# Kernel tuning notes

Hardware: AMD Instinct MI355X
Metric: run time of the kernel (lower is better)

Reference implementation:

```python
import jax, jax.numpy as jnp
import numpy as np

HIGH, LOW = 768, 384
LOW2 = LOW // 2  # PNL uses low_dim // reduc_ratio, reduc_ratio=2
B, N = 8, 4096
EPS = 1e-5


def _nl_block(x_h, x_l, wg, bg, wt, bt, wp, bp, ww, bw, gamma, beta):
    # x_h: [B,N,H], x_l: [B,N0,H]; conv1x1 == per-token linear
    Nl = x_l.shape[1]
    g = jnp.einsum('bnc,dc->bnd', x_l, wg) + bg      # [B,N0,D]
    th = jnp.einsum('bnc,dc->bnd', x_h, wt) + bt     # [B,N,D]
    ph = jnp.einsum('bnc,dc->bnd', x_l, wp) + bp     # [B,N0,D]
    # attention = (th @ ph^T) / N0; y = attention @ g. Reassociate:
    kv = jnp.einsum('bnd,bne->bde', ph, g) / Nl      # [B,D,D]
    y = jnp.einsum('bnd,bde->bne', th, kv)           # [B,N,D]
    y = jnp.einsum('bnd,cd->bnc', y, ww) + bw        # [B,N,H]
    # BatchNorm1d over channel dim, training-mode batch stats (biased var)
    mu = y.mean(axis=(0, 1))
    var = y.var(axis=(0, 1))
    y = (y - mu) * jax.lax.rsqrt(var + EPS) * gamma + beta
    return y + x_h


def setup_inputs() -> dict:
    key = jax.random.key(0)
    ks = jax.random.split(key, 24)
    s = 0.02
    d = {
        'x': jax.random.normal(ks[0], (B, N, HIGH), jnp.float32),
        'x0': jax.random.normal(ks[1], (B, N, HIGH), jnp.float32),
        # CNL params (low_dim = 384)
        'c_wg': s * jax.random.normal(ks[2], (LOW, HIGH)), 'c_bg': s * jax.random.normal(ks[3], (LOW,)),
        'c_wt': s * jax.random.normal(ks[4], (LOW, HIGH)), 'c_bt': s * jax.random.normal(ks[5], (LOW,)),
        'c_wp': s * jax.random.normal(ks[6], (LOW, HIGH)), 'c_bp': s * jax.random.normal(ks[7], (LOW,)),
        'c_ww': s * jax.random.normal(ks[8], (HIGH, LOW)), 'c_bw': s * jax.random.normal(ks[9], (HIGH,)),
        'c_gamma': 1.0 + 0.1 * jax.random.normal(ks[10], (HIGH,)),
        'c_beta': s * jax.random.normal(ks[11], (HIGH,)),
        # PNL params (low_dim // 2 = 192)
        'p_wg': s * jax.random.normal(ks[12], (LOW2, HIGH)), 'p_bg': s * jax.random.normal(ks[13], (LOW2,)),
        'p_wt': s * jax.random.normal(ks[14], (LOW2, HIGH)), 'p_bt': s * jax.random.normal(ks[15], (LOW2,)),
        'p_wp': s * jax.random.normal(ks[16], (LOW2, HIGH)), 'p_bp': s * jax.random.normal(ks[17], (LOW2,)),
        'p_ww': s * jax.random.normal(ks[18], (HIGH, LOW2)), 'p_bw': s * jax.random.normal(ks[19], (HIGH,)),
        'p_gamma': 1.0 + 0.1 * jax.random.normal(ks[20], (HIGH,)),
        'p_beta': s * jax.random.normal(ks[21], (HIGH,)),
    }
    return d


def reference(x, x0,
              c_wg, c_bg, c_wt, c_bt, c_wp, c_bp, c_ww, c_bw, c_gamma, c_beta,
              p_wg, p_bg, p_wt, p_bt, p_wp, p_bp, p_ww, p_bw, p_gamma, p_beta):
    z = _nl_block(x, x0, c_wg, c_bg, c_wt, c_bt, c_wp, c_bp, c_ww, c_bw, c_gamma, c_beta)
    out = _nl_block(z, x0, p_wg, p_bg, p_wt, p_bt, p_wp, p_bp, p_ww, p_bw, p_gamma, p_beta)
    return out
```

## Files before the change

kernel.cpp:

```cpp
#include <hip/hip_runtime.h>
#include <stdint.h>

typedef unsigned short u16;
typedef __bf16 bf16x8 __attribute__((ext_vector_type(8)));
typedef short s16x8 __attribute__((ext_vector_type(8)));
typedef short s16x4 __attribute__((ext_vector_type(4)));
typedef float f32x4 __attribute__((ext_vector_type(4)));

__device__ __forceinline__ u16 f2bf(float f) {
  uint32_t u = __builtin_bit_cast(uint32_t, f);
  u += 0x7fffu + ((u >> 16) & 1u);
  return (u16)(u >> 16);
}
__device__ __forceinline__ float bf2f(u16 h) {
  uint32_t u = ((uint32_t)h) << 16;
  return __builtin_bit_cast(float, u);
}

__device__ __forceinline__ void gl16(const u16* g, u16* l) {
  __builtin_amdgcn_global_load_lds(
      (const __attribute__((address_space(1))) void*)g,
      (__attribute__((address_space(3))) void*)l, 16, 0, 0);
}

__device__ __forceinline__ void barf() {
  asm volatile("s_barrier" ::: "memory");
}

__device__ __forceinline__ int src_chunk(int l) {
  return (((l & 3) ^ ((l >> 3) & 3)) * 8);
}
__device__ __forceinline__ int rd_koff(int l) {
  return (((l >> 4) ^ (((l & 15) >> 1) & 3)) * 8);
}

__global__ void cvt_in2(const float* __restrict__ a, const float* __restrict__ b,
                        u16* __restrict__ da, u16* __restrict__ db, long n8each) {
  long stride = (long)gridDim.x * blockDim.x;
  long total = 2 * n8each;
  for (long i = (long)blockIdx.x * blockDim.x + threadIdx.x; i < total; i += stride) {
    const float* src = (i < n8each) ? a + i * 8 : b + (i - n8each) * 8;
    u16* dst = (i < n8each) ? da + i * 8 : db + (i - n8each) * 8;
    const f32x4* s = (const f32x4*)src;
    f32x4 v0 = s[0], v1 = s[1];
    s16x8 o;
#pragma unroll
    for (int j = 0; j < 4; ++j) o[j] = (short)f2bf(v0[j]);
#pragma unroll
    for (int j = 0; j < 4; ++j) o[4 + j] = (short)f2bf(v1[j]);
    *(s16x8*)dst = o;
  }
}

__global__ void cvt_flat8(const float* __restrict__ src, u16* __restrict__ dst,
                          long n8, float scale) {
  long stride = (long)gridDim.x * blockDim.x;
  for (long i = (long)blockIdx.x * blockDim.x + threadIdx.x; i < n8; i += stride) {
    const f32x4* s = (const f32x4*)(src + i * 8);
    f32x4 a = s[0], b = s[1];
    s16x8 o;
#pragma unroll
    for (int j = 0; j < 4; ++j) o[j] = (short)f2bf(a[j] * scale);
#pragma unroll
    for (int j = 0; j < 4; ++j) o[4 + j] = (short)f2bf(b[j] * scale);
    *(s16x8*)(dst + i * 8) = o;
  }
}

__global__ void prep_w(const float* __restrict__ c_wg, const float* __restrict__ c_wp,
                       const float* __restrict__ p_wg, const float* __restrict__ p_wp,
                       const float* __restrict__ c_wt, const float* __restrict__ p_wt,
                       const float* __restrict__ c_ww, const float* __restrict__ p_ww,
                       u16* __restrict__ wcat, u16* __restrict__ wt_c,
                       u16* __restrict__ wt_p, u16* __restrict__ ww_c,
                       u16* __restrict__ ww_p) {
  const int C0 = 1280 * 768 / 4;
  const int C1 = C0 + 384 * 768 / 4;
  const int C2 = C1 + 256 * 768 / 4;
  const int C3 = C2 + 768 * 384 / 4;
  const int C4 = C3 + 768 * 256 / 4;
  int stride = gridDim.x * blockDim.x;
  for (int i = blockIdx.x * blockDim.x + threadIdx.x; i < C4; i += stride) {
    const float* src = nullptr;
    u16* dst;
    if (i < C0) {
      int e = i * 4;
      dst = wcat + e;
      int r = e / 768;
      if (r < 384) src = c_wg + e;
      else if (r < 768) src = c_wp + e - 384 * 768;
      else if (r < 960) src = p_wg + e - 768 * 768;
      else if (r < 1024) src = nullptr;
      else if (r < 1216) src = p_wp + e - 1024 * 768;
      else src = nullptr;
    } else if (i < C1) {
      int e = (i - C0) * 4; dst = wt_c + e; src = c_wt + e;
    } else if (i < C2) {
      int e = (i - C1) * 4; dst = wt_p + e;
      src = (e / 768 < 192) ? p_wt + e : nullptr;
    } else if (i < C3) {
      int e = (i - C2) * 4; dst = ww_c + e; src = c_ww + e;
    } else {
      int e = (i - C3) * 4; dst = ww_p + e;
      int r = e >> 8, c = e & 255;
      src = (c < 192) ? p_ww + r * 192 + c : nullptr;
    }
    s16x4 o;
    if (src) {
      f32x4 v = *(const f32x4*)src;
#pragma unroll
      for (int j = 0; j < 4; ++j) o[j] = (short)f2bf(v[j]);
    } else {
      o = s16x4{0, 0, 0, 0};
    }
    *(s16x4*)dst = o;
  }
}

__global__ void prep_b(const float* __restrict__ c_bg, const float* __restrict__ c_bp,
                       const float* __restrict__ p_bg, const float* __restrict__ p_bp,
                       const float* __restrict__ c_bt, const float* __restrict__ p_bt,
                       float* __restrict__ biasb, float* __restrict__ sums) {
  int i = blockIdx.x * blockDim.x + threadIdx.x;
  if (i < 1920) {
    float v = 0.f;
    if (i < 384) v = c_bg[i];
    else if (i < 768) v = c_bp[i - 384];
    else if (i < 960) v = p_bg[i - 768];
    else if (i < 1024) v = 0.f;
    else if (i < 1216) v = p_bp[i - 1024];
    else if (i < 1280) v = 0.f;
    else if (i < 1664) v = c_bt[i - 1280];
    else if (i < 1856) v = p_bt[i - 1664];
    biasb[i] = v;
  } else if (i < 1920 + 3072) {
    sums[i - 1920] = 0.f;
  }
}

template <int BIAS, int SUMS>
__global__ __launch_bounds__(512) void gemm_nt_big(
    const u16* __restrict__ A, const u16* __restrict__ B, void* __restrict__ Cv,
    const float* __restrict__ bias, float* __restrict__ sums,
    int ntiles, long lda, long ldb, long ldc, int K,
    long aBatch, long bBatch, long cBatch) {
  __shared__ u16 As[4][256 * 32];
  __shared__ u16 Bs[4][256 * 32];

  const int bm = blockIdx.x / ntiles;
  const int bn = blockIdx.x % ntiles;
  const int bb = blockIdx.y;
  const int nt = K >> 5;

  const u16* Ab = A + (long)bb * aBatch + (long)bm * 256 * lda;
  const u16* Bb = B + (long)bb * bBatch + (long)bn * 256 * ldb;

  const int t = threadIdx.x;
  const int w = t >> 6;
  const int l = t & 63;
  const int wr = w >> 2;
  const int wc = w & 3;

  const int srow = w * 16 + (l >> 2);
  const int cg = src_chunk(l);
  const long aoff0 = (long)srow * lda + cg;
  const long aoff1 = (long)(128 + srow) * lda + cg;
  const long boff0 = (long)srow * ldb + cg;
  const long boff1 = (long)(128 + srow) * ldb + cg;

#define STAGE_A(T, BUF)                                   \
  gl16(Ab + aoff0 + (long)(T) * 32, &As[BUF][w * 512]);   \
  gl16(Ab + aoff1 + (long)(T) * 32, &As[BUF][(8 + w) * 512]);
#define STAGE_B(T, BUF)                                   \
  gl16(Bb + boff0 + (long)(T) * 32, &Bs[BUF][w * 512]);   \
  gl16(Bb + boff1 + (long)(T) * 32, &Bs[BUF][(8 + w) * 512]);

  f32x4 acc[8][4] = {};

  STAGE_A(0, 0); STAGE_B(0, 0);
  if (nt > 1) { STAGE_A(1, 1); STAGE_B(1, 1); }
  if (nt > 2) { STAGE_A(2, 2); STAGE_B(2, 2); }
  if (nt > 2)      asm volatile("s_waitcnt vmcnt(8)" ::: "memory");
  else if (nt > 1) asm volatile("s_waitcnt vmcnt(4)" ::: "memory");
  else             asm volatile("s_waitcnt vmcnt(0)" ::: "memory");
  barf();

  const int koff = rd_koff(l);
  const int ar = wr * 128 + (l & 15);
  const int br = wc * 64 + (l & 15);

  for (int tt = 0; tt < nt; ++tt) {
    const int cur = tt & 3;
    const int pf = (tt + 3) & 3;
    const bool do_pf = (tt + 3) < nt;

    bf16x8 bfr[4], af[4];
#pragma unroll
    for (int ni = 0; ni < 4; ++ni)
      bfr[ni] = __builtin_bit_cast(
          bf16x8, *(const s16x8*)(&Bs[cur][(br + ni * 16) * 32 + koff]));
#pragma unroll
    for (int mi = 0; mi < 4; ++mi)
      af[mi] = __builtin_bit_cast(
          bf16x8, *(const s16x8*)(&As[cur][(ar + mi * 16) * 32 + koff]));
    if (do_pf) { STAGE_A(tt + 3, pf); }
    barf();
    __builtin_amdgcn_s_setprio(1);
#pragma unroll
    for (int mi = 0; mi < 4; ++mi)
#pragma unroll
      for (int ni = 0; ni < 4; ++ni)
        acc[mi][ni] = __builtin_amdgcn_mfma_f32_16x16x32_bf16(
            af[mi], bfr[ni], acc[mi][ni], 0, 0, 0);
    __builtin_amdgcn_s_setprio(0);
    barf();

    bf16x8 ag[4];
#pragma unroll
    for (int mi = 0; mi < 4; ++mi)
      ag[mi] = __builtin_bit_cast(
          bf16x8, *(const s16x8*)(&As[cur][(ar + 64 + mi * 16) * 32 + koff]));
    if (do_pf) { STAGE_B(tt + 3, pf); }
    barf();
    __builtin_amdgcn_s_setprio(1);
#pragma unroll
    for (int mi = 0; mi < 4; ++mi)
#pragma unroll
      for (int ni = 0; ni < 4; ++ni)
        acc[4 + mi][ni] = __builtin_amdgcn_mfma_f32_16x16x32_bf16(
            ag[mi], bfr[ni], acc[4 + mi][ni], 0, 0, 0);
    __builtin_amdgcn_s_setprio(0);
    if (tt + 4 <= nt)      asm volatile("s_waitcnt vmcnt(8)" ::: "memory");
    else if (tt + 3 == nt) asm volatile("s_waitcnt vmcnt(4)" ::: "memory");
    else if (tt + 2 == nt) asm volatile("s_waitcnt vmcnt(0)" ::: "memory");
    barf();
  }
#undef STAGE_A
#undef STAGE_B
  __builtin_amdgcn_sched_barrier(0);

  const long crow0 = (long)bm * 256 + wr * 128;
  const long ccol0 = (long)bn * 256 + wc * 64;
  u16* C = (u16*)Cv + (long)bb * cBatch;
#pragma unroll
  for (int mi = 0; mi < 8; ++mi)
#pragma unroll
    for (int j = 0; j < 4; ++j) {
      long row = crow0 + mi * 16 + (l >> 4) * 4 + j;
      float rb = (BIAS == 1) ? bias[row] : 0.f;
#pragma unroll
      for (int ni = 0; ni < 4; ++ni) {
        long col = ccol0 + ni * 16 + (l & 15);
        C[row * ldc + col] = f2bf(acc[mi][ni][j] + rb);
      }
    }

  if (SUMS) {
#pragma unroll
    for (int ni = 0; ni < 4; ++ni) {
      float s = 0.f, q = 0.f;
#pragma unroll
      for (int mi = 0; mi < 8; ++mi)
#pragma unroll
        for (int j = 0; j < 4; ++j) {
          float v = acc[mi][ni][j];
          s += v;
          q += v * v;
        }
      s += __shfl_xor(s, 16);
      q += __shfl_xor(q, 16);
      s += __shfl_xor(s, 32);
      q += __shfl_xor(q, 32);
      if (l < 16) {
        long col = ccol0 + ni * 16 + l;
        atomicAdd(&sums[col], s);
        atomicAdd(&sums[768 + col], q);
      }
    }
  }
}

template <int BIAS, int OUT_ATOMIC, int SUMS>
__global__ __launch_bounds__(256) void gemm_nt(
    const u16* __restrict__ A, const u16* __restrict__ B, void* __restrict__ Cv,
    const float* __restrict__ bias, float* __restrict__ sums,
    int ntiles, long lda, long ldb, long ldc, int K,
    long aBatch, long bBatch, long cBatch) {
  __shared__ u16 As[2][128 * 32];
  __shared__ u16 Bs[2][128 * 32];

  const int bm = blockIdx.x / ntiles;
  const int bn = blockIdx.x % ntiles;
  const int bb = blockIdx.y;
  const int kChunk = K / gridDim.z;
  const long k0base = (long)blockIdx.z * kChunk;
  const int nt = kChunk >> 5;

  const u16* Ab = A + (long)bb * aBatch + (long)bm * 128 * lda + k0base;
  const u16* Bb = B + (long)bb * bBatch + (long)bn * 128 * ldb + k0base;

  const int t = threadIdx.x;
  const int w = t >> 6;
  const int l = t & 63;
  const int wr = w >> 1, wc = w & 1;

  const int cg = src_chunk(l);
  const long aoff = (long)(32 * w + (l >> 2)) * lda + cg;
  const long boff = (long)(32 * w + (l >> 2)) * ldb + cg;

  f32x4 acc[4][4] = {};

  gl16(Ab + aoff, &As[0][(32 * w) * 32]);
  gl16(Ab + aoff + 16 * lda, &As[0][(32 * w + 16) * 32]);
  gl16(Bb + boff, &Bs[0][(32 * w) * 32]);
  gl16(Bb + boff + 16 * ldb, &Bs[0][(32 * w + 16) * 32]);
  if (nt > 1) {
    gl16(Ab + aoff + 32, &As[1][(32 * w) * 32]);
    gl16(Ab + aoff + 16 * lda + 32, &As[1][(32 * w + 16) * 32]);
    gl16(Bb + boff + 32, &Bs[1][(32 * w) * 32]);
    gl16(Bb + boff + 16 * ldb + 32, &Bs[1][(32 * w + 16) * 32]);
  }

  const int koff = rd_koff(l);

  for (int tt = 0; tt < nt; ++tt) {
    const int cur = tt & 1;
    if (tt + 1 < nt)
      asm volatile("s_waitcnt vmcnt(4)" ::: "memory");
    else
      asm volatile("s_waitcnt vmcnt(0)" ::: "memory");
    __builtin_amdgcn_s_barrier();

    bf16x8 af[4], bfr[4];
#pragma unroll
    for (int mi = 0; mi < 4; ++mi)
      af[mi] = __builtin_bit_cast(
          bf16x8, *(const s16x8*)(&As[cur][(wr * 64 + mi * 16 + (l & 15)) * 32 + koff]));
#pragma unroll
    for (int ni = 0; ni < 4; ++ni)
      bfr[ni] = __builtin_bit_cast(
          bf16x8, *(const s16x8*)(&Bs[cur][(wc * 64 + ni * 16 + (l & 15)) * 32 + koff]));
#pragma unroll
    for (int mi = 0; mi < 4; ++mi)
#pragma unroll
      for (int ni = 0; ni < 4; ++ni)
        acc[mi][ni] = __builtin_amdgcn_mfma_f32_16x16x32_bf16(
            af[mi], bfr[ni], acc[mi][ni], 0, 0, 0);

    __builtin_amdgcn_s_barrier();
    if (tt + 2 < nt) {
      const long ko = (long)(tt + 2) * 32;
      gl16(Ab + aoff + ko, &As[cur][(32 * w) * 32]);
      gl16(Ab + aoff + 16 * lda + ko, &As[cur][(32 * w + 16) * 32]);
      gl16(Bb + boff + ko, &Bs[cur][(32 * w) * 32]);
      gl16(Bb + boff + 16 * ldb + ko, &Bs[cur][(32 * w + 16) * 32]);
    }
  }
  __builtin_amdgcn_sched_barrier(0);

  const long crow0 = (long)bm * 128 + wr * 64;
  const long ccol0 = (long)bn * 128 + wc * 64;

  if (OUT_ATOMIC) {
    float* C = (float*)Cv + (long)bb * cBatch;
#pragma unroll
    for (int mi = 0; mi < 4; ++mi)
#pragma unroll
      for (int j = 0; j < 4; ++j) {
        long row = crow0 + mi * 16 + (l >> 4) * 4 + j;
#pragma unroll
        for (int ni = 0; ni < 4; ++ni) {
          long col = ccol0 + ni * 16 + (l & 15);
          atomicAdd(&C[row * ldc + col], acc[mi][ni][j]);
        }
      }
  } else {
    u16* C = (u16*)Cv + (long)bb * cBatch;
#pragma unroll
    for (int mi = 0; mi < 4; ++mi)
#pragma unroll
      for (int j = 0; j < 4; ++j) {
        long row = crow0 + mi * 16 + (l >> 4) * 4 + j;
        float rb = (BIAS == 1) ? bias[row] : 0.f;
#pragma unroll
        for (int ni = 0; ni < 4; ++ni) {
          long col = ccol0 + ni * 16 + (l & 15);
          float cb = (BIAS == 2) ? bias[col] : 0.f;
          C[row * ldc + col] = f2bf(acc[mi][ni][j] + rb + cb);
        }
      }
  }

  if (SUMS) {
#pragma unroll
    for (int ni = 0; ni < 4; ++ni) {
      float s = 0.f, q = 0.f;
#pragma unroll
      for (int mi = 0; mi < 4; ++mi)
#pragma unroll
        for (int j = 0; j < 4; ++j) {
          float v = acc[mi][ni][j];
          s += v;
          q += v * v;
        }
      s += __shfl_xor(s, 16);
      q += __shfl_xor(q, 16);
      s += __shfl_xor(s, 32);
      q += __shfl_xor(q, 32);
      if (l < 16) {
        long col = ccol0 + ni * 16 + l;
        atomicAdd(&sums[col], s);
        atomicAdd(&sums[768 + col], q);
      }
    }
  }
}

__global__ void bn_stats(const float* __restrict__ sums, const float* __restrict__ gamma,
                         const float* __restrict__ beta, float* __restrict__ stats,
                         float invN) {
  int c = threadIdx.x;
  float mu = sums[c] * invN;
  float var = sums[768 + c] * invN - mu * mu;
  float sc = gamma[c] * rsqrtf(var + 1e-5f);
  stats[c] = sc;
  stats[768 + c] = beta[c] - mu * sc;
}

template <int OUT_F32>
__global__ void bn_apply(const u16* __restrict__ pre, const u16* __restrict__ resid,
                         const float* __restrict__ stats, void* __restrict__ out,
                         long n8) {
  long stride = (long)gridDim.x * blockDim.x;
  for (long i = (long)blockIdx.x * blockDim.x + threadIdx.x; i < n8; i += stride) {
    long base = i * 8;
    int c = (int)(base % 768);
    f32x4 sc0 = *(const f32x4*)(stats + c);
    f32x4 sc1 = *(const f32x4*)(stats + c + 4);
    f32x4 sh0 = *(const f32x4*)(stats + 768 + c);
    f32x4 sh1 = *(const f32x4*)(stats + 768 + c + 4);
    s16x8 p = *(const s16x8*)(pre + base);
    s16x8 rv = *(const s16x8*)(resid + base);
    float o[8];
#pragma unroll
    for (int j = 0; j < 4; ++j)
      o[j] = bf2f((u16)p[j]) * sc0[j] + sh0[j] + bf2f((u16)rv[j]);
#pragma unroll
    for (int j = 0; j < 4; ++j)
      o[4 + j] = bf2f((u16)p[4 + j]) * sc1[j] + sh1[j] + bf2f((u16)rv[4 + j]);
    if (OUT_F32) {
      f32x4 o0, o1;
#pragma unroll
      for (int j = 0; j < 4; ++j) { o0[j] = o[j]; o1[j] = o[4 + j]; }
      f32x4* op = (f32x4*)((float*)out + base);
      op[0] = o0;
      op[1] = o1;
    } else {
      s16x8 ov;
#pragma unroll
      for (int j = 0; j < 8; ++j) ov[j] = (short)f2bf(o[j]);
      *(s16x8*)((u16*)out + base) = ov;
    }
  }
}

extern "C" void kernel_launch(void* const* d_in, const int* in_sizes, int n_in,
                              void* d_out, int out_size, void* d_ws, size_t ws_size,
                              hipStream_t stream) {
  const float* x = (const float*)d_in[0];
  const float* x0 = (const float*)d_in[1];
  const float* c_wg = (const float*)d_in[2];
  const float* c_bg = (const float*)d_in[3];
  const float* c_wt = (const float*)d_in[4];
  const float* c_bt = (const float*)d_in[5];
  const float* c_wp = (const float*)d_in[6];
  const float* c_bp = (const float*)d_in[7];
  const float* c_ww = (const float*)d_in[8];
  const float* c_gamma = (const float*)d_in[10];
  const float* c_beta = (const float*)d_in[11];
  const float* p_wg = (const float*)d_in[12];
  const float* p_bg = (const float*)d_in[13];
  const float* p_wt = (const float*)d_in[14];
  const float* p_bt = (const float*)d_in[15];
  const float* p_wp = (const float*)d_in[16];
  const float* p_bp = (const float*)d_in[17];
  const float* p_ww = (const float*)d_in[18];
  const float* p_gamma = (const float*)d_in[20];
  const float* p_beta = (const float*)d_in[21];

  char* ws = (char*)d_ws;
  const long NT = 32768;
  u16* xbf = (u16*)(ws + 0);
  u16* x0bf = (u16*)(ws + 50331648);
  u16* th = (u16*)(ws + 50331648);
  float* kvf_c = (float*)(ws + 75497472);
  float* kvf_p = (float*)(ws + 80216064);
  u16* kvb = (u16*)(ws + 82313216);
  u16* kvwT = (u16*)(ws + 84672512);
  u16* gphT = (u16*)(ws + 100663296);
  u16* wcat = (u16*)(ws + 184549376);
  u16* wt_c = (u16*)(ws + 186515456);
  u16* wt_p = (u16*)(ws + 187105280);
  u16* ww_c = (u16*)(ws + 187498496);
  u16* ww_p = (u16*)(ws + 188088320);
  float* biasb = (float*)(ws + 188481536);
  float* sums = (float*)(ws + 188489216);
  float* stats = (float*)(ws + 188501504);
  u16* zbf = xbf;
  u16* pre = gphT;

  cvt_in2<<<4096, 256, 0, stream>>>(x, x0, xbf, x0bf, NT * 768 / 8);
  prep_w<<<480, 256, 0, stream>>>(c_wg, c_wp, p_wg, p_wp, c_wt, p_wt, c_ww, p_ww,
                                  wcat, wt_c, wt_p, ww_c, ww_p);
  prep_b<<<20, 256, 0, stream>>>(c_bg, c_bp, p_bg, p_bp, c_bt, p_bt, biasb, sums);

  gemm_nt_big<1, 0><<<dim3(5 * 128, 1, 1), 512, 0, stream>>>(
      wcat, x0bf, gphT, biasb, nullptr, 128, 768, 768, 32768, 768, 0, 0, 0);
  hipMemsetAsync(kvf_c, 0, 4718592 + 2097152, stream);

  gemm_nt<2, 0, 0><<<dim3(256 * 3, 1, 1), 256, 0, stream>>>(
      xbf, wt_c, th, biasb + 1280, nullptr, 3, 768, 768, 384, 768, 0, 0, 0);
  gemm_nt<0, 1, 0><<<dim3(9, 8, 8), 256, 0, stream>>>(
      gphT + (long)384 * 32768, gphT, kvf_c, nullptr, nullptr, 3, 32768, 32768,
      384, 4096, 4096, 4096, (long)384 * 384);
  cvt_flat8<<<576, 256, 0, stream>>>(kvf_c, kvb, (long)8 * 384 * 384 / 8, 1.f / 4096.f);
  gemm_nt<0, 0, 0><<<dim3(18, 8, 1), 256, 0, stream>>>(
      ww_c, kvb, kvwT, nullptr, nullptr, 3, 384, 384, 384, 384, 0,
      (long)384 * 384, (long)768 * 384);
  gemm_nt_big<0, 1><<<dim3(48, 8, 1), 512, 0, stream>>>(
      th, kvwT, pre, nullptr, sums, 3, 384, 384, 768, 384, (long)4096 * 384,
      (long)768 * 384, (long)4096 * 768);
  bn_stats<<<1, 768, 0, stream>>>(sums, c_gamma, c_beta, stats, 1.f / 32768.f);
  bn_apply<0><<<2048, 256, 0, stream>>>(pre, xbf, stats, zbf, NT * 768 / 8);

  gemm_nt<2, 0, 0><<<dim3(256 * 2, 1, 1), 256, 0, stream>>>(
      zbf, wt_p, th, biasb + 1664, nullptr, 2, 768, 768, 256, 768, 0, 0, 0);
  gemm_nt<0, 1, 0><<<dim3(4, 8, 8), 256, 0, stream>>>(
      gphT + (long)1024 * 32768, gphT + (long)768 * 32768, kvf_p, nullptr, nullptr,
      2, 32768, 32768, 256, 4096, 4096, 4096, (long)256 * 256);
  cvt_flat8<<<256, 256, 0, stream>>>(kvf_p, kvb, (long)8 * 256 * 256 / 8, 1.f / 4096.f);
  gemm_nt<0, 0, 0><<<dim3(12, 8, 1), 256, 0, stream>>>(
      ww_p, kvb, kvwT, nullptr, nullptr, 2, 256, 256, 256, 256, 0,
      (long)256 * 256, (long)768 * 256);
  gemm_nt_big<0, 1><<<dim3(48, 8, 1), 512, 0, stream>>>(
      th, kvwT, pre, nullptr, sums + 1536, 3, 256, 256, 768, 256, (long)4096 * 256,
      (long)768 * 256, (long)4096 * 768);
  bn_stats<<<1, 768, 0, stream>>>(sums + 1536, p_gamma, p_beta, stats, 1.f / 32768.f);
  bn_apply<1><<<2048, 256, 0, stream>>>(pre, zbf, stats, (float*)d_out, NT * 768 / 8);
}
```

Measured before the change: 450.0 us.

## Restructure GEMM prefetch pipelines and replicate BN stat accumulators

The big GEMM now does one wait-plus-barrier per K-step and issues the A and B prefetch together at the top, instead of two half-steps each fenced by barriers. The small GEMM moves from a 2-stage to a 3-stage LDS ring so the prefetch issues right after the barrier with no trailing barrier, and it raises wave priority around its MFMAs. BatchNorm sum atomics are spread over 8 replicas keyed by block index to cut atomic contention, and bn_stats sums the replicas. The trade-off is more LDS and registers (8 A fragments held at once) and a larger zeroed sums buffer.

```diff
diff --git a/kernel.cpp b/kernel.cpp
--- a/kernel.cpp
+++ b/kernel.cpp
@@ -133,7 +133,7 @@
     else if (i < 1664) v = c_bt[i - 1280];
     else if (i < 1856) v = p_bt[i - 1664];
     biasb[i] = v;
-  } else if (i < 1920 + 3072) {
+  } else if (i < 1920 + 24576) {
     sums[i - 1920] = 0.f;
   }
 }
@@ -180,10 +180,6 @@
   STAGE_A(0, 0); STAGE_B(0, 0);
   if (nt > 1) { STAGE_A(1, 1); STAGE_B(1, 1); }
   if (nt > 2) { STAGE_A(2, 2); STAGE_B(2, 2); }
-  if (nt > 2)      asm volatile("s_waitcnt vmcnt(8)" ::: "memory");
-  else if (nt > 1) asm volatile("s_waitcnt vmcnt(4)" ::: "memory");
-  else             asm volatile("s_waitcnt vmcnt(0)" ::: "memory");
-  barf();
 
   const int koff = rd_koff(l);
   const int ar = wr * 128 + (l & 15);
@@ -191,49 +187,35 @@
 
   for (int tt = 0; tt < nt; ++tt) {
     const int cur = tt & 3;
-    const int pf = (tt + 3) & 3;
-    const bool do_pf = (tt + 3) < nt;
-
-    bf16x8 bfr[4], af[4];
+    const int ahead = nt - 1 - tt;
+    if (ahead >= 2)      asm volatile("s_waitcnt vmcnt(8)" ::: "memory");
+    else if (ahead == 1) asm volatile("s_waitcnt vmcnt(4)" ::: "memory");
+    else                 asm volatile("s_waitcnt vmcnt(0)" ::: "memory");
+    barf();
+
+    if (tt + 3 < nt) {
+      const int pf = (tt + 3) & 3;
+      STAGE_A(tt + 3, pf);
+      STAGE_B(tt + 3, pf);
+    }
+
+    bf16x8 bfr[4], af[8];
 #pragma unroll
     for (int ni = 0; ni < 4; ++ni)
       bfr[ni] = __builtin_bit_cast(
           bf16x8, *(const s16x8*)(&Bs[cur][(br + ni * 16) * 32 + koff]));
 #pragma unroll
-    for (int mi = 0; mi < 4; ++mi)
+    for (int mi = 0; mi < 8; ++mi)
       af[mi] = __builtin_bit_cast(
           bf16x8, *(const s16x8*)(&As[cur][(ar + mi * 16) * 32 + koff]));
-    if (do_pf) { STAGE_A(tt + 3, pf); }
-    barf();
     __builtin_amdgcn_s_setprio(1);
 #pragma unroll
-    for (int mi = 0; mi < 4; ++mi)
+    for (int mi = 0; mi < 8; ++mi)
 #pragma unroll
       for (int ni = 0; ni < 4; ++ni)
         acc[mi][ni] = __builtin_amdgcn_mfma_f32_16x16x32_bf16(
             af[mi], bfr[ni], acc[mi][ni], 0, 0, 0);
     __builtin_amdgcn_s_setprio(0);
-    barf();
-
-    bf16x8 ag[4];
-#pragma unroll
-    for (int mi = 0; mi < 4; ++mi)
-      ag[mi] = __builtin_bit_cast(
-          bf16x8, *(const s16x8*)(&As[cur][(ar + 64 + mi * 16) * 32 + koff]));
-    if (do_pf) { STAGE_B(tt + 3, pf); }
-    barf();
-    __builtin_amdgcn_s_setprio(1);
-#pragma unroll
-    for (int mi = 0; mi < 4; ++mi)
-#pragma unroll
-      for (int ni = 0; ni < 4; ++ni)
-        acc[4 + mi][ni] = __builtin_amdgcn_mfma_f32_16x16x32_bf16(
-            ag[mi], bfr[ni], acc[4 + mi][ni], 0, 0, 0);
-    __builtin_amdgcn_s_setprio(0);
-    if (tt + 4 <= nt)      asm volatile("s_waitcnt vmcnt(8)" ::: "memory");
-    else if (tt + 3 == nt) asm volatile("s_waitcnt vmcnt(4)" ::: "memory");
-    else if (tt + 2 == nt) asm volatile("s_waitcnt vmcnt(0)" ::: "memory");
-    barf();
   }
 #undef STAGE_A
 #undef STAGE_B
@@ -256,6 +238,7 @@
     }
 
   if (SUMS) {
+    float* srep = sums + (blockIdx.x & 7) * 1536;
 #pragma unroll
     for (int ni = 0; ni < 4; ++ni) {
       float s = 0.f, q = 0.f;
@@ -273,8 +256,8 @@
       q += __shfl_xor(q, 32);
       if (l < 16) {
         long col = ccol0 + ni * 16 + l;
-        atomicAdd(&sums[col], s);
-        atomicAdd(&sums[768 + col], q);
+        atomicAdd(&srep[col], s);
+        atomicAdd(&srep[768 + col], q);
       }
     }
   }
@@ -286,8 +269,8 @@
     const float* __restrict__ bias, float* __restrict__ sums,
     int ntiles, long lda, long ldb, long ldc, int K,
     long aBatch, long bBatch, long cBatch) {
-  __shared__ u16 As[2][128 * 32];
-  __shared__ u16 Bs[2][128 * 32];
+  __shared__ u16 As[3][128 * 32];
+  __shared__ u16 Bs[3][128 * 32];
 
   const int bm = blockIdx.x / ntiles;
   const int bn = blockIdx.x % ntiles;
@@ -310,26 +293,29 @@
 
   f32x4 acc[4][4] = {};
 
-  gl16(Ab + aoff, &As[0][(32 * w) * 32]);
-  gl16(Ab + aoff + 16 * lda, &As[0][(32 * w + 16) * 32]);
-  gl16(Bb + boff, &Bs[0][(32 * w) * 32]);
-  gl16(Bb + boff + 16 * ldb, &Bs[0][(32 * w + 16) * 32]);
-  if (nt > 1) {
-    gl16(Ab + aoff + 32, &As[1][(32 * w) * 32]);
-    gl16(Ab + aoff + 16 * lda + 32, &As[1][(32 * w + 16) * 32]);
-    gl16(Bb + boff + 32, &Bs[1][(32 * w) * 32]);
-    gl16(Bb + boff + 16 * ldb + 32, &Bs[1][(32 * w + 16) * 32]);
-  }
+#define STG(T, BUF)                                          \
+  gl16(Ab + aoff + (long)(T) * 32, &As[BUF][(32 * w) * 32]); \
+  gl16(Ab + aoff + 16 * lda + (long)(T) * 32, &As[BUF][(32 * w + 16) * 32]); \
+  gl16(Bb + boff + (long)(T) * 32, &Bs[BUF][(32 * w) * 32]); \
+  gl16(Bb + boff + 16 * ldb + (long)(T) * 32, &Bs[BUF][(32 * w + 16) * 32]);
+
+  STG(0, 0);
+  if (nt > 1) { STG(1, 1); }
 
   const int koff = rd_koff(l);
 
   for (int tt = 0; tt < nt; ++tt) {
-    const int cur = tt & 1;
+    const int cur = tt % 3;
     if (tt + 1 < nt)
       asm volatile("s_waitcnt vmcnt(4)" ::: "memory");
     else
       asm volatile("s_waitcnt vmcnt(0)" ::: "memory");
-    __builtin_amdgcn_s_barrier();
+    barf();
+
+    if (tt + 2 < nt) {
+      const int pf = (tt + 2) % 3;
+      STG(tt + 2, pf);
+    }
 
     bf16x8 af[4], bfr[4];
 #pragma unroll
@@ -340,22 +326,16 @@
     for (int ni = 0; ni < 4; ++ni)
       bfr[ni] = __builtin_bit_cast(
           bf16x8, *(const s16x8*)(&Bs[cur][(wc * 64 + ni * 16 + (l & 15)) * 32 + koff]));
+    __builtin_amdgcn_s_setprio(1);
 #pragma unroll
     for (int mi = 0; mi < 4; ++mi)
 #pragma unroll
       for (int ni = 0; ni < 4; ++ni)
         acc[mi][ni] = __builtin_amdgcn_mfma_f32_16x16x32_bf16(
             af[mi], bfr[ni], acc[mi][ni], 0, 0, 0);
-
-    __builtin_amdgcn_s_barrier();
-    if (tt + 2 < nt) {
-      const long ko = (long)(tt + 2) * 32;
-      gl16(Ab + aoff + ko, &As[cur][(32 * w) * 32]);
-      gl16(Ab + aoff + 16 * lda + ko, &As[cur][(32 * w + 16) * 32]);
-      gl16(Bb + boff + ko, &Bs[cur][(32 * w) * 32]);
-      gl16(Bb + boff + 16 * ldb + ko, &Bs[cur][(32 * w + 16) * 32]);
-    }
-  }
+    __builtin_amdgcn_s_setprio(0);
+  }
+#undef STG
   __builtin_amdgcn_sched_barrier(0);
 
   const long crow0 = (long)bm * 128 + wr * 64;
@@ -392,6 +372,7 @@
   }
 
   if (SUMS) {
+    float* srep = sums + (blockIdx.x & 7) * 1536;
 #pragma unroll
     for (int ni = 0; ni < 4; ++ni) {
       float s = 0.f, q = 0.f;
@@ -409,8 +390,8 @@
       q += __shfl_xor(q, 32);
       if (l < 16) {
         long col = ccol0 + ni * 16 + l;
-        atomicAdd(&sums[col], s);
-        atomicAdd(&sums[768 + col], q);
+        atomicAdd(&srep[col], s);
+        atomicAdd(&srep[768 + col], q);
       }
     }
   }
@@ -420,8 +401,14 @@
                          const float* __restrict__ beta, float* __restrict__ stats,
                          float invN) {
   int c = threadIdx.x;
-  float mu = sums[c] * invN;
-  float var = sums[768 + c] * invN - mu * mu;
+  float s = 0.f, q = 0.f;
+#pragma unroll
+  for (int r = 0; r < 8; ++r) {
+    s += sums[r * 1536 + c];
+    q += sums[r * 1536 + 768 + c];
+  }
+  float mu = s * invN;
+  float var = q * invN - mu * mu;
   float sc = gamma[c] * rsqrtf(var + 1e-5f);
   stats[c] = sc;
   stats[768 + c] = beta[c] - mu * sc;
@@ -505,14 +492,14 @@
   u16* ww_p = (u16*)(ws + 188088320);
   float* biasb = (float*)(ws + 188481536);
   float* sums = (float*)(ws + 188489216);
-  float* stats = (float*)(ws + 188501504);
+  float* stats = (float*)(ws + 188587520);
   u16* zbf = xbf;
   u16* pre = gphT;
 
   cvt_in2<<<4096, 256, 0, stream>>>(x, x0, xbf, x0bf, NT * 768 / 8);
   prep_w<<<480, 256, 0, stream>>>(c_wg, c_wp, p_wg, p_wp, c_wt, p_wt, c_ww, p_ww,
                                   wcat, wt_c, wt_p, ww_c, ww_p);
-  prep_b<<<20, 256, 0, stream>>>(c_bg, c_bp, p_bg, p_bp, c_bt, p_bt, biasb, sums);
+  prep_b<<<104, 256, 0, stream>>>(c_bg, c_bp, p_bg, p_bp, c_bt, p_bt, biasb, sums);
 
   gemm_nt_big<1, 0><<<dim3(5 * 128, 1, 1), 512, 0, stream>>>(
       wcat, x0bf, gphT, biasb, nullptr, 128, 768, 768, 32768, 768, 0, 0, 0);
@@ -543,8 +530,8 @@
       ww_p, kvb, kvwT, nullptr, nullptr, 2, 256, 256, 256, 256, 0,
       (long)256 * 256, (long)768 * 256);
   gemm_nt_big<0, 1><<<dim3(48, 8, 1), 512, 0, stream>>>(
-      th, kvwT, pre, nullptr, sums + 1536, 3, 256, 256, 768, 256, (long)4096 * 256,
-      (long)768 * 256, (long)4096 * 768);
-  bn_stats<<<1, 768, 0, stream>>>(sums + 1536, p_gamma, p_beta, stats, 1.f / 32768.f);
+      th, kvwT, pre, nullptr, sums + 8 * 1536, 3, 256, 256, 768, 256,
+      (long)4096 * 256, (long)768 * 256, (long)4096 * 768);
+  bn_stats<<<1, 768, 0, stream>>>(sums + 8 * 1536, p_gamma, p_beta, stats, 1.f / 32768.f);
   bn_apply<1><<<2048, 256, 0, stream>>>(pre, zbf, stats, (float*)d_out, NT * 768 / 8);
 }
```

After: 470.9 us. +4.6%, slower.

## Swap MFMA operands for row-contiguous vector stores and replicate BN sum atomics

Applied to the files above, without the earlier changes.

Swaps the A/B operands of the MFMA calls so each lane holds four consecutive output columns of one row. The epilogues can then write 8-byte packed bf16 vectors instead of scalar 2-byte stores, and atomic adds to the kv accumulator become contiguous per lane. BatchNorm partial sums are spread over 8 replicas chosen by block index to reduce atomic contention, and bn_stats adds the replicas back together. This needs a larger zeroed sums region, a moved stats buffer and more shuffle steps in the sums reduction.

```diff
diff --git a/kernel.cpp b/kernel.cpp
--- a/kernel.cpp
+++ b/kernel.cpp
@@ -133,7 +133,7 @@
     else if (i < 1664) v = c_bt[i - 1280];
     else if (i < 1856) v = p_bt[i - 1664];
     biasb[i] = v;
-  } else if (i < 1920 + 3072) {
+  } else if (i < 1920 + 24576) {
     sums[i - 1920] = 0.f;
   }
 }
@@ -211,7 +211,7 @@
 #pragma unroll
       for (int ni = 0; ni < 4; ++ni)
         acc[mi][ni] = __builtin_amdgcn_mfma_f32_16x16x32_bf16(
-            af[mi], bfr[ni], acc[mi][ni], 0, 0, 0);
+            bfr[ni], af[mi], acc[mi][ni], 0, 0, 0);
     __builtin_amdgcn_s_setprio(0);
     barf();
 
@@ -228,7 +228,7 @@
 #pragma unroll
       for (int ni = 0; ni < 4; ++ni)
         acc[4 + mi][ni] = __builtin_amdgcn_mfma_f32_16x16x32_bf16(
-            ag[mi], bfr[ni], acc[4 + mi][ni], 0, 0, 0);
+            bfr[ni], ag[mi], acc[4 + mi][ni], 0, 0, 0);
     __builtin_amdgcn_s_setprio(0);
     if (tt + 4 <= nt)      asm volatile("s_waitcnt vmcnt(8)" ::: "memory");
     else if (tt + 3 == nt) asm volatile("s_waitcnt vmcnt(4)" ::: "memory");
@@ -243,38 +243,47 @@
   const long ccol0 = (long)bn * 256 + wc * 64;
   u16* C = (u16*)Cv + (long)bb * cBatch;
 #pragma unroll
-  for (int mi = 0; mi < 8; ++mi)
-#pragma unroll
-    for (int j = 0; j < 4; ++j) {
-      long row = crow0 + mi * 16 + (l >> 4) * 4 + j;
-      float rb = (BIAS == 1) ? bias[row] : 0.f;
-#pragma unroll
-      for (int ni = 0; ni < 4; ++ni) {
-        long col = ccol0 + ni * 16 + (l & 15);
-        C[row * ldc + col] = f2bf(acc[mi][ni][j] + rb);
-      }
-    }
+  for (int mi = 0; mi < 8; ++mi) {
+    long row = crow0 + mi * 16 + (l & 15);
+    float rb = (BIAS == 1) ? bias[row] : 0.f;
+    u16* Cr = C + row * ldc + ccol0 + (l >> 4) * 4;
+#pragma unroll
+    for (int ni = 0; ni < 4; ++ni) {
+      s16x4 v;
+#pragma unroll
+      for (int j = 0; j < 4; ++j) v[j] = (short)f2bf(acc[mi][ni][j] + rb);
+      *(s16x4*)(Cr + ni * 16) = v;
+    }
+  }
 
   if (SUMS) {
+    float* srep = sums + (blockIdx.x & 7) * 1536;
 #pragma unroll
     for (int ni = 0; ni < 4; ++ni) {
-      float s = 0.f, q = 0.f;
+      f32x4 s = {}, q = {};
 #pragma unroll
       for (int mi = 0; mi < 8; ++mi)
 #pragma unroll
         for (int j = 0; j < 4; ++j) {
           float v = acc[mi][ni][j];
-          s += v;
-          q += v * v;
+          s[j] += v;
+          q[j] += v * v;
         }
-      s += __shfl_xor(s, 16);
-      q += __shfl_xor(q, 16);
-      s += __shfl_xor(s, 32);
-      q += __shfl_xor(q, 32);
-      if (l < 16) {
-        long col = ccol0 + ni * 16 + l;
-        atomicAdd(&sums[col], s);
-        atomicAdd(&sums[768 + col], q);
+#pragma unroll
+      for (int m = 1; m < 16; m <<= 1) {
+#pragma unroll
+        for (int j = 0; j < 4; ++j) {
+          s[j] += __shfl_xor(s[j], m);
+          q[j] += __shfl_xor(q[j], m);
+        }
+      }
+      if ((l & 15) == 0) {
+        long cb = ccol0 + ni * 16 + (l >> 4) * 4;
+#pragma unroll
+        for (int j = 0; j < 4; ++j) {
+          atomicAdd(&srep[cb + j], s[j]);
+          atomicAdd(&srep[768 + cb + j], q[j]);
+        }
       }
     }
   }
@@ -345,7 +354,7 @@
 #pragma unroll
       for (int ni = 0; ni < 4; ++ni)
         acc[mi][ni] = __builtin_amdgcn_mfma_f32_16x16x32_bf16(
-            af[mi], bfr[ni], acc[mi][ni], 0, 0, 0);
+            bfr[ni], af[mi], acc[mi][ni], 0, 0, 0);
 
     __builtin_amdgcn_s_barrier();
     if (tt + 2 < nt) {
@@ -364,53 +373,65 @@
   if (OUT_ATOMIC) {
     float* C = (float*)Cv + (long)bb * cBatch;
 #pragma unroll
-    for (int mi = 0; mi < 4; ++mi)
-#pragma unroll
-      for (int j = 0; j < 4; ++j) {
-        long row = crow0 + mi * 16 + (l >> 4) * 4 + j;
-#pragma unroll
-        for (int ni = 0; ni < 4; ++ni) {
-          long col = ccol0 + ni * 16 + (l & 15);
-          atomicAdd(&C[row * ldc + col], acc[mi][ni][j]);
+    for (int mi = 0; mi < 4; ++mi) {
+      long row = crow0 + mi * 16 + (l & 15);
+#pragma unroll
+      for (int ni = 0; ni < 4; ++ni) {
+        long cb = ccol0 + ni * 16 + (l >> 4) * 4;
+#pragma unroll
+        for (int j = 0; j < 4; ++j)
+          atomicAdd(&C[row * ldc + cb + j], acc[mi][ni][j]);
+      }
+    }
+  } else {
+    u16* C = (u16*)Cv + (long)bb * cBatch;
+#pragma unroll
+    for (int mi = 0; mi < 4; ++mi) {
+      long row = crow0 + mi * 16 + (l & 15);
+      float rb = (BIAS == 1) ? bias[row] : 0.f;
+      u16* Cr = C + row * ldc + ccol0 + (l >> 4) * 4;
+#pragma unroll
+      for (int ni = 0; ni < 4; ++ni) {
+        f32x4 cbv = {};
+        if (BIAS == 2)
+          cbv = *(const f32x4*)(bias + ccol0 + ni * 16 + (l >> 4) * 4);
+        s16x4 v;
+#pragma unroll
+        for (int j = 0; j < 4; ++j)
+          v[j] = (short)f2bf(acc[mi][ni][j] + rb + cbv[j]);
+        *(s16x4*)(Cr + ni * 16) = v;
+      }
+    }
+  }
+
+  if (SUMS) {
+    float* srep = sums + (blockIdx.x & 7) * 1536;
+#pragma unroll
+    for (int ni = 0; ni < 4; ++ni) {
+      f32x4 s = {}, q = {};
+#pragma unroll
+      for (int mi = 0; mi < 4; ++mi)
+#pragma unroll
+        for (int j = 0; j < 4; ++j) {
+          float v = acc[mi][ni][j];
+          s[j] += v;
+          q[j] += v * v;
+        }
+#pragma unroll
+      for (int m = 1; m < 16; m <<= 1) {
+#pragma unroll
+        for (int j = 0; j < 4; ++j) {
+          s[j] += __shfl_xor(s[j], m);
+          q[j] += __shfl_xor(q[j], m);
         }
       }
-  } else {
-    u16* C = (u16*)Cv + (long)bb * cBatch;
-#pragma unroll
-    for (int mi = 0; mi < 4; ++mi)
-#pragma unroll
-      for (int j = 0; j < 4; ++j) {
-        long row = crow0 + mi * 16 + (l >> 4) * 4 + j;
-        float rb = (BIAS == 1) ? bias[row] : 0.f;
-#pragma unroll
-        for (int ni = 0; ni < 4; ++ni) {
-          long col = ccol0 + ni * 16 + (l & 15);
-          float cb = (BIAS == 2) ? bias[col] : 0.f;
-          C[row * ldc + col] = f2bf(acc[mi][ni][j] + rb + cb);
+      if ((l & 15) == 0) {
+        long cb = ccol0 + ni * 16 + (l >> 4) * 4;
+#pragma unroll
+        for (int j = 0; j < 4; ++j) {
+          atomicAdd(&srep[cb + j], s[j]);
+          atomicAdd(&srep[768 + cb + j], q[j]);
         }
-      }
-  }
-
-  if (SUMS) {
-#pragma unroll
-    for (int ni = 0; ni < 4; ++ni) {
-      float s = 0.f, q = 0.f;
-#pragma unroll
-      for (int mi = 0; mi < 4; ++mi)
-#pragma unroll
-        for (int j = 0; j < 4; ++j) {
-          float v = acc[mi][ni][j];
-          s += v;
-          q += v * v;
-        }
-      s += __shfl_xor(s, 16);
-      q += __shfl_xor(q, 16);
-      s += __shfl_xor(s, 32);
-      q += __shfl_xor(q, 32);
-      if (l < 16) {
-        long col = ccol0 + ni * 16 + l;
-        atomicAdd(&sums[col], s);
-        atomicAdd(&sums[768 + col], q);
       }
     }
   }
@@ -420,8 +441,14 @@
                          const float* __restrict__ beta, float* __restrict__ stats,
                          float invN) {
   int c = threadIdx.x;
-  float mu = sums[c] * invN;
-  float var = sums[768 + c] * invN - mu * mu;
+  float s = 0.f, q = 0.f;
+#pragma unroll
+  for (int r = 0; r < 8; ++r) {
+    s += sums[r * 1536 + c];
+    q += sums[r * 1536 + 768 + c];
+  }
+  float mu = s * invN;
+  float var = q * invN - mu * mu;
   float sc = gamma[c] * rsqrtf(var + 1e-5f);
   stats[c] = sc;
   stats[768 + c] = beta[c] - mu * sc;
@@ -505,14 +532,14 @@
   u16* ww_p = (u16*)(ws + 188088320);
   float* biasb = (float*)(ws + 188481536);
   float* sums = (float*)(ws + 188489216);
-  float* stats = (float*)(ws + 188501504);
+  float* stats = (float*)(ws + 188587520);
   u16* zbf = xbf;
   u16* pre = gphT;
 
   cvt_in2<<<4096, 256, 0, stream>>>(x, x0, xbf, x0bf, NT * 768 / 8);
   prep_w<<<480, 256, 0, stream>>>(c_wg, c_wp, p_wg, p_wp, c_wt, p_wt, c_ww, p_ww,
                                   wcat, wt_c, wt_p, ww_c, ww_p);
-  prep_b<<<20, 256, 0, stream>>>(c_bg, c_bp, p_bg, p_bp, c_bt, p_bt, biasb, sums);
+  prep_b<<<104, 256, 0, stream>>>(c_bg, c_bp, p_bg, p_bp, c_bt, p_bt, biasb, sums);
 
   gemm_nt_big<1, 0><<<dim3(5 * 128, 1, 1), 512, 0, stream>>>(
       wcat, x0bf, gphT, biasb, nullptr, 128, 768, 768, 32768, 768, 0, 0, 0);
@@ -543,8 +570,8 @@
       ww_p, kvb, kvwT, nullptr, nullptr, 2, 256, 256, 256, 256, 0,
       (long)256 * 256, (long)768 * 256);
   gemm_nt_big<0, 1><<<dim3(48, 8, 1), 512, 0, stream>>>(
-      th, kvwT, pre, nullptr, sums + 1536, 3, 256, 256, 768, 256, (long)4096 * 256,
-      (long)768 * 256, (long)4096 * 768);
-  bn_stats<<<1, 768, 0, stream>>>(sums + 1536, p_gamma, p_beta, stats, 1.f / 32768.f);
+      th, kvwT, pre, nullptr, sums + 8 * 1536, 3, 256, 256, 768, 256,
+      (long)4096 * 256, (long)768 * 256, (long)4096 * 768);
+  bn_stats<<<1, 768, 0, stream>>>(sums + 8 * 1536, p_gamma, p_beta, stats, 1.f / 32768.f);
   bn_apply<1><<<2048, 256, 0, stream>>>(pre, zbf, stats, (float*)d_out, NT * 768 / 8);
 }
```

Result: slower. 621.0 us (+38.0%).
